# Optimization experiments

Measured on AMD Instinct MI355X. Metric: run time of the kernel, lower is better.

## Reference

```python
import jax, jax.numpy as jnp
import numpy as np

NUM_GROUPS = 32
EPS = 1e-5  # torch GroupNorm default


def group_norm(x, gamma, beta):
    # x: [b, c, h, w]
    b, c, h, w = x.shape
    xg = x.reshape(b, NUM_GROUPS, c // NUM_GROUPS, h, w)
    mean = xg.mean(axis=(2, 3, 4), keepdims=True)
    var = xg.var(axis=(2, 3, 4), keepdims=True)
    xg = (xg - mean) * jax.lax.rsqrt(var + EPS)
    x = xg.reshape(b, c, h, w)
    return x * gamma[None, :, None, None] + beta[None, :, None, None]


def conv1x1(x, w, bias):
    # 1x1 conv == channel matmul. x: [b,c,h,w], w: [cout,cin]
    y = jnp.einsum('bchw,dc->bdhw', x, w)
    return y + bias[None, :, None, None]


def setup_inputs() -> dict:
    key = jax.random.key(0)
    ks = jax.random.split(key, 11)
    C = 512
    scale = 1.0 / np.sqrt(C)
    x = jax.random.normal(ks[0], (4, C, 64, 64), dtype=jnp.float32)
    return {
        'x': x,
        'gamma': jnp.ones((C,), jnp.float32),
        'beta': jnp.zeros((C,), jnp.float32),
        'wq': jax.random.uniform(ks[1], (C, C), jnp.float32, -scale, scale),
        'bq': jax.random.uniform(ks[2], (C,), jnp.float32, -scale, scale),
        'wk': jax.random.uniform(ks[3], (C, C), jnp.float32, -scale, scale),
        'bk': jax.random.uniform(ks[4], (C,), jnp.float32, -scale, scale),
        'wv': jax.random.uniform(ks[5], (C, C), jnp.float32, -scale, scale),
        'bv': jax.random.uniform(ks[6], (C,), jnp.float32, -scale, scale),
        'wo': jax.random.uniform(ks[7], (C, C), jnp.float32, -scale, scale),
        'bo': jax.random.uniform(ks[8], (C,), jnp.float32, -scale, scale),
    }


def reference(x, gamma, beta, wq, bq, wk, bk, wv, bv, wo, bo):
    b, c, h, w = x.shape
    h_ = group_norm(x, gamma, beta)
    q = conv1x1(h_, wq, bq).reshape(b, c, h * w)
    k = conv1x1(h_, wk, bk).reshape(b, c, h * w)
    v = conv1x1(h_, wv, bv).reshape(b, c, h * w)
    # scores: [b, hw, hw] -- q^T k scaled by c^-0.5
    scores = jnp.einsum('bcn,bcm->bnm', q, k) * (c ** -0.5)
    attn = jax.nn.softmax(scores, axis=2)
    # h_ = v @ attn^T : [b, c, hw]
    out = jnp.einsum('bcm,bnm->bcn', v, attn).reshape(b, c, h, w)
    return x + conv1x1(out, wo, bo)
```

## Files before the change

kernel.cpp:

```cpp
#include <hip/hip_runtime.h>

typedef __bf16 bf16x8 __attribute__((ext_vector_type(8)));
typedef __bf16 bf16x4 __attribute__((ext_vector_type(4)));
typedef float floatx4 __attribute__((ext_vector_type(4)));

#define AS1(p) ((const __attribute__((address_space(1))) unsigned int*)(p))
#define AS3(p) ((__attribute__((address_space(3))) unsigned int*)(p))

__device__ __forceinline__ void async_cp16(const void* g, void* l) {
  __builtin_amdgcn_global_load_lds(AS1(g), AS3(l), 16, 0, 0);
}


template <bool OUT_F32>
__global__ __launch_bounds__(256, 2) void gemm_bt(
    const __bf16* __restrict__ A, const __bf16* __restrict__ B,
    void* __restrict__ Cv, const float* __restrict__ bias,
    const float* __restrict__ residual, const float* __restrict__ colscale,
    int lda, int ldb, int ldc, long sA, long sB, long sC, long sR, int K,
    int bias_mode, float scale, int swz) {
  __shared__ alignas(16) __bf16 As[128 * 64];
  __shared__ alignas(16) __bf16 Bs[128 * 64];

  const int t = threadIdx.x;
  const int bz = blockIdx.z;
  int bx = blockIdx.x, by = blockIdx.y;
  if (swz) {
    const int xcd = bx & 7, idx = bx >> 3;
    by = xcd + (idx >> 2) * 8;
    bx = idx & 3;
  }
  const int m0 = by * 128;
  const int n0 = bx * 128;

  const __bf16* Ab = A + (size_t)bz * sA;
  const __bf16* Bb = B + (size_t)bz * sB;

  const int sr = t >> 3;
  const int sc = ((t & 7) ^ ((t >> 3) & 7)) * 8;
  const __bf16* gA0 = Ab + (size_t)(m0 + sr) * lda + sc;
  const __bf16* gA1 = gA0 + (size_t)32 * lda;
  const __bf16* gA2 = gA0 + (size_t)64 * lda;
  const __bf16* gA3 = gA0 + (size_t)96 * lda;
  const __bf16* gB0 = Bb + (size_t)(n0 + sr) * ldb + sc;
  const __bf16* gB1 = gB0 + (size_t)32 * ldb;
  const __bf16* gB2 = gB0 + (size_t)64 * ldb;
  const __bf16* gB3 = gB0 + (size_t)96 * ldb;
  __bf16* lA0 = &As[t * 8];
  __bf16* lA1 = &As[(t + 256) * 8];
  __bf16* lA2 = &As[(t + 512) * 8];
  __bf16* lA3 = &As[(t + 768) * 8];
  __bf16* lB0 = &Bs[t * 8];
  __bf16* lB1 = &Bs[(t + 256) * 8];
  __bf16* lB2 = &Bs[(t + 512) * 8];
  __bf16* lB3 = &Bs[(t + 768) * 8];

  const int lane = t & 63;
  const int wv = t >> 6;
  const int wm = (wv & 1) * 64;
  const int wn = (wv >> 1) * 64;
  const int l15 = lane & 15;
  const int kg = lane >> 4;
  const int l7 = l15 & 7;

  int aoff0[4], boff0[4], aoff1[4], boff1[4];
#pragma unroll
  for (int i = 0; i < 4; ++i) {
    aoff0[i] = (wm + i * 16 + l15) * 64 + (kg ^ l7) * 8;
    aoff1[i] = (wm + i * 16 + l15) * 64 + ((4 + kg) ^ l7) * 8;
  }
#pragma unroll
  for (int j = 0; j < 4; ++j) {
    boff0[j] = (wn + j * 16 + l15) * 64 + (kg ^ l7) * 8;
    boff1[j] = (wn + j * 16 + l15) * 64 + ((4 + kg) ^ l7) * 8;
  }

  floatx4 acc[4][4] = {};

  const int KT = K >> 6;
  for (int kt = 0; kt < KT; ++kt) {
    const size_t ko = (size_t)kt * 64;
    async_cp16(gA0 + ko, lA0);
    async_cp16(gA1 + ko, lA1);
    async_cp16(gA2 + ko, lA2);
    async_cp16(gA3 + ko, lA3);
    async_cp16(gB0 + ko, lB0);
    async_cp16(gB1 + ko, lB1);
    async_cp16(gB2 + ko, lB2);
    async_cp16(gB3 + ko, lB3);
    __syncthreads();
    bf16x8 af[4], bfr[4];
#pragma unroll
    for (int i = 0; i < 4; ++i) af[i] = *(const bf16x8*)&As[aoff0[i]];
#pragma unroll
    for (int j = 0; j < 4; ++j) bfr[j] = *(const bf16x8*)&Bs[boff0[j]];
#pragma unroll
    for (int i = 0; i < 4; ++i)
#pragma unroll
      for (int j = 0; j < 4; ++j)
        acc[i][j] = __builtin_amdgcn_mfma_f32_16x16x32_bf16(af[i], bfr[j],
                                                            acc[i][j], 0, 0, 0);
#pragma unroll
    for (int i = 0; i < 4; ++i) af[i] = *(const bf16x8*)&As[aoff1[i]];
#pragma unroll
    for (int j = 0; j < 4; ++j) bfr[j] = *(const bf16x8*)&Bs[boff1[j]];
#pragma unroll
    for (int i = 0; i < 4; ++i)
#pragma unroll
      for (int j = 0; j < 4; ++j)
        acc[i][j] = __builtin_amdgcn_mfma_f32_16x16x32_bf16(af[i], bfr[j],
                                                            acc[i][j], 0, 0, 0);
    __syncthreads();
  }

  const int r0 = m0 + wm + (kg << 2);
  const int c0 = n0 + wn + l15;
#pragma unroll
  for (int i = 0; i < 4; ++i) {
#pragma unroll
    for (int r = 0; r < 4; ++r) {
      const int row = r0 + i * 16 + r;
      float brow = 0.f;
      if (bias_mode == 1) brow = bias[row];
#pragma unroll
      for (int j = 0; j < 4; ++j) {
        const int col = c0 + j * 16;
        float v = acc[i][j][r];
        if (OUT_F32 && colscale) v *= colscale[(size_t)bz * 4096 + col];
        if (bias_mode == 1) v += brow;
        v *= scale;
        const size_t off = (size_t)row * ldc + col;
        if (OUT_F32) {
          float* Cf = (float*)Cv + (size_t)bz * sC;
          if (residual) v += residual[(size_t)bz * sR + off];
          Cf[off] = v;
        } else {
          __bf16* Cb = (__bf16*)Cv + (size_t)bz * sC;
          Cb[off] = (__bf16)v;
        }
      }
    }
  }
}

__global__ __launch_bounds__(256, 2) void gemm_small(
    const __bf16* __restrict__ A0, const __bf16* __restrict__ B0,
    __bf16* __restrict__ C0, const __bf16* __restrict__ A1,
    const __bf16* __restrict__ B1, __bf16* __restrict__ C1, float scale0) {
  __shared__ alignas(16) __bf16 As[128 * 32];
  __shared__ alignas(16) __bf16 Bs[128 * 32];

  const int t = threadIdx.x;
  const int z = blockIdx.z;
  const __bf16* A = z ? A1 : A0;
  const __bf16* B = z ? B1 : B0;
  __bf16* C = z ? C1 : C0;
  const float scale = z ? 1.0f : scale0;
  const int m0 = blockIdx.y * 128;
  const int n0 = blockIdx.x * 128;

  const int sr = t >> 2;
  const int sc = (t & 3) ^ ((t >> 3) & 3);
  const __bf16* gA0 = A + (size_t)(m0 + sr) * 512 + sc * 8;
  const __bf16* gA1 = gA0 + (size_t)64 * 512;
  const __bf16* gB0 = B + (size_t)(n0 + sr) * 512 + sc * 8;
  const __bf16* gB1 = gB0 + (size_t)64 * 512;
  __bf16* lA0 = &As[t * 8];
  __bf16* lA1 = &As[(t + 256) * 8];
  __bf16* lB0 = &Bs[t * 8];
  __bf16* lB1 = &Bs[(t + 256) * 8];

  const int lane = t & 63;
  const int wvv = t >> 6;
  const int wm = (wvv & 1) * 64;
  const int wn = (wvv >> 1) * 64;
  const int l15 = lane & 15;
  const int kg = lane >> 4;

  const int kgs = (kg ^ ((l15 >> 1) & 3)) * 8;
  int aoff[4], boff[4];
#pragma unroll
  for (int i = 0; i < 4; ++i) aoff[i] = (wm + i * 16 + l15) * 32 + kgs;
#pragma unroll
  for (int j = 0; j < 4; ++j) boff[j] = (wn + j * 16 + l15) * 32 + kgs;

  floatx4 acc[4][4] = {};

  for (int kt = 0; kt < 16; ++kt) {
    const size_t ko = (size_t)kt * 32;
    async_cp16(gA0 + ko, lA0);
    async_cp16(gA1 + ko, lA1);
    async_cp16(gB0 + ko, lB0);
    async_cp16(gB1 + ko, lB1);
    __syncthreads();
    bf16x8 af[4], bfr[4];
#pragma unroll
    for (int i = 0; i < 4; ++i) af[i] = *(const bf16x8*)&As[aoff[i]];
#pragma unroll
    for (int j = 0; j < 4; ++j) bfr[j] = *(const bf16x8*)&Bs[boff[j]];
#pragma unroll
    for (int i = 0; i < 4; ++i)
#pragma unroll
      for (int j = 0; j < 4; ++j)
        acc[i][j] = __builtin_amdgcn_mfma_f32_16x16x32_bf16(af[i], bfr[j],
                                                            acc[i][j], 0, 0, 0);
    __syncthreads();
  }

  const int r0 = m0 + wm + (kg << 2);
  const int c0 = n0 + wn + l15;
#pragma unroll
  for (int i = 0; i < 4; ++i)
#pragma unroll
    for (int r = 0; r < 4; ++r) {
      const int row = r0 + i * 16 + r;
#pragma unroll
      for (int j = 0; j < 4; ++j)
        C[(size_t)row * 512 + c0 + j * 16] = (__bf16)(acc[i][j][r] * scale);
    }
}

__global__ __launch_bounds__(256, 2) void gemm_qk(
    const __bf16* __restrict__ G, const __bf16* __restrict__ Ht,
    const float* __restrict__ wvec, const float* __restrict__ sred,
    const float* __restrict__ gn2, __bf16* __restrict__ SP,
    float* __restrict__ Lpart) {
  __shared__ alignas(16) __bf16 As[128 * 64];
  __shared__ alignas(16) __bf16 Bs[128 * 64];
  __shared__ float smq[128];
  __shared__ float smf[256];

  const int t = threadIdx.x;
  const int bz = blockIdx.z;
  const int m0 = blockIdx.x * 128;
  const int n0 = blockIdx.y * 128;
  const long sH = 2097152;

  const __bf16* Ab = G + (size_t)bz * sH;
  const __bf16* Bb = Ht + (size_t)bz * sH;

  const int sr = t >> 3;
  const int sc = ((t & 7) ^ ((t >> 3) & 7)) * 8;
  const __bf16* gA0 = Ab + (size_t)(n0 + sr) * 512 + sc;
  const __bf16* gA1 = gA0 + (size_t)32 * 512;
  const __bf16* gA2 = gA0 + (size_t)64 * 512;
  const __bf16* gA3 = gA0 + (size_t)96 * 512;
  const __bf16* gB0 = Bb + (size_t)(m0 + sr) * 512 + sc;
  const __bf16* gB1 = gB0 + (size_t)32 * 512;
  const __bf16* gB2 = gB0 + (size_t)64 * 512;
  const __bf16* gB3 = gB0 + (size_t)96 * 512;
  __bf16* lA0 = &As[t * 8];
  __bf16* lA1 = &As[(t + 256) * 8];
  __bf16* lA2 = &As[(t + 512) * 8];
  __bf16* lA3 = &As[(t + 768) * 8];
  __bf16* lB0 = &Bs[t * 8];
  __bf16* lB1 = &Bs[(t + 256) * 8];
  __bf16* lB2 = &Bs[(t + 512) * 8];
  __bf16* lB3 = &Bs[(t + 768) * 8];

  const int lane = t & 63;
  const int wv = t >> 6;
  const int wm = (wv & 1) * 64;
  const int wn = (wv >> 1) * 64;
  const int l15 = lane & 15;
  const int kg = lane >> 4;
  const int l7 = l15 & 7;

  if (t < 128) {
    smq[t] = sqrtf(gn2[(size_t)bz * 4096 + n0 + t]) * sqrtf(sred[0]) + sred[1];
  }

  int aoff0[4], boff0[4], aoff1[4], boff1[4];
#pragma unroll
  for (int i = 0; i < 4; ++i) {
    aoff0[i] = (wm + i * 16 + l15) * 64 + (kg ^ l7) * 8;
    aoff1[i] = (wm + i * 16 + l15) * 64 + ((4 + kg) ^ l7) * 8;
  }
#pragma unroll
  for (int j = 0; j < 4; ++j) {
    boff0[j] = (wn + j * 16 + l15) * 64 + (kg ^ l7) * 8;
    boff1[j] = (wn + j * 16 + l15) * 64 + ((4 + kg) ^ l7) * 8;
  }

  floatx4 acc[4][4] = {};

  for (int kt = 0; kt < 8; ++kt) {
    const size_t ko = (size_t)kt * 64;
    async_cp16(gA0 + ko, lA0);
    async_cp16(gA1 + ko, lA1);
    async_cp16(gA2 + ko, lA2);
    async_cp16(gA3 + ko, lA3);
    async_cp16(gB0 + ko, lB0);
    async_cp16(gB1 + ko, lB1);
    async_cp16(gB2 + ko, lB2);
    async_cp16(gB3 + ko, lB3);
    __syncthreads();
    bf16x8 af[4], bfr[4];
#pragma unroll
    for (int i = 0; i < 4; ++i) af[i] = *(const bf16x8*)&As[aoff0[i]];
#pragma unroll
    for (int j = 0; j < 4; ++j) bfr[j] = *(const bf16x8*)&Bs[boff0[j]];
#pragma unroll
    for (int i = 0; i < 4; ++i)
#pragma unroll
      for (int j = 0; j < 4; ++j)
        acc[i][j] = __builtin_amdgcn_mfma_f32_16x16x32_bf16(af[i], bfr[j],
                                                            acc[i][j], 0, 0, 0);
#pragma unroll
    for (int i = 0; i < 4; ++i) af[i] = *(const bf16x8*)&As[aoff1[i]];
#pragma unroll
    for (int j = 0; j < 4; ++j) bfr[j] = *(const bf16x8*)&Bs[boff1[j]];
#pragma unroll
    for (int i = 0; i < 4; ++i)
#pragma unroll
      for (int j = 0; j < 4; ++j)
        acc[i][j] = __builtin_amdgcn_mfma_f32_16x16x32_bf16(af[i], bfr[j],
                                                            acc[i][j], 0, 0, 0);
    __syncthreads();
  }

  float wv4[4];
#pragma unroll
  for (int j = 0; j < 4; ++j)
    wv4[j] = wvec[(size_t)bz * 4096 + m0 + wn + j * 16 + l15];

  __bf16* Sb = SP + (size_t)bz * 16777216;
  const int wnh = wv >> 1;
#pragma unroll
  for (int i = 0; i < 4; ++i) {
#pragma unroll
    for (int r = 0; r < 4; ++r) {
      const int rl = wm + i * 16 + (kg << 2) + r;
      const float Mh = smq[rl];
      const size_t rowbase = (size_t)(n0 + rl) * 4096 + m0 + wn;
      float se = 0.f;
#pragma unroll
      for (int j = 0; j < 4; ++j) {
        const float p = __expf(acc[i][j][r] + wv4[j] - Mh);
        se += p;
        Sb[rowbase + j * 16 + l15] = (__bf16)p;
      }
#pragma unroll
      for (int off = 1; off < 16; off <<= 1) se += __shfl_xor(se, off);
      if (l15 == 0) smf[wnh * 128 + rl] = se;
    }
  }
  __syncthreads();
  if (t < 128)
    Lpart[((size_t)bz * 4096 + n0 + t) * 32 + blockIdx.x] =
        smf[t] + smf[128 + t];
}

__global__ __launch_bounds__(256) void gnorm_kernel(const __bf16* __restrict__ G,
                                                    float* __restrict__ gn2) {
  const int t = threadIdx.x;
  const int row = blockIdx.x * 4 + (t >> 6);
  const int lane = t & 63;
  const bf16x8 g = *(const bf16x8*)(G + (size_t)row * 512 + lane * 8);
  float n2 = 0.f;
#pragma unroll
  for (int k = 0; k < 8; ++k) {
    const float f = (float)g[k];
    n2 += f * f;
  }
#pragma unroll
  for (int off = 32; off; off >>= 1) n2 += __shfl_down(n2, off);
  if (lane == 0) gn2[row] = n2;
}

__global__ __launch_bounds__(256) void lsum_kernel(const float* __restrict__ Lp,
                                                   float* __restrict__ invL) {
  const int row = blockIdx.x * 256 + threadIdx.x;
  const float* p = Lp + (size_t)row * 32;
  float L = 0.f;
#pragma unroll
  for (int j = 0; j < 32; ++j) L += p[j];
  invL[row] = 1.0f / L;
}

__global__ __launch_bounds__(256) void reduce_kernel(
    const float* __restrict__ hn2, const float* __restrict__ wvec,
    float* __restrict__ sred) {
  const int t = threadIdx.x;
  const floatx4* h4 = (const floatx4*)hn2;
  const floatx4* w4 = (const floatx4*)wvec;
  float mh = 0.f, mw = -1e30f;
  for (int i = t; i < 4096; i += 256) {
    const floatx4 a = h4[i], b = w4[i];
#pragma unroll
    for (int k = 0; k < 4; ++k) {
      mh = fmaxf(mh, a[k]);
      mw = fmaxf(mw, b[k]);
    }
  }
#pragma unroll
  for (int off = 32; off; off >>= 1) {
    mh = fmaxf(mh, __shfl_down(mh, off));
    mw = fmaxf(mw, __shfl_down(mw, off));
  }
  __shared__ float red[8];
  if ((t & 63) == 0) {
    red[t >> 6] = mh;
    red[4 + (t >> 6)] = mw;
  }
  __syncthreads();
  if (t == 0) {
    sred[0] = fmaxf(fmaxf(red[0], red[1]), fmaxf(red[2], red[3]));
    sred[1] = fmaxf(fmaxf(red[4], red[5]), fmaxf(red[6], red[7]));
  }
}

__global__ __launch_bounds__(256) void gn_stats(const float* __restrict__ x,
                                                float* __restrict__ part) {
  const int t = threadIdx.x;
  const size_t base = (size_t)blockIdx.x * 8192;
  const floatx4* xp = (const floatx4*)(x + base);
  float s = 0.f, ss = 0.f;
#pragma unroll
  for (int i = 0; i < 8; ++i) {
    floatx4 v = xp[t + i * 256];
#pragma unroll
    for (int k = 0; k < 4; ++k) {
      s += v[k];
      ss += v[k] * v[k];
    }
  }
#pragma unroll
  for (int off = 32; off; off >>= 1) {
    s += __shfl_down(s, off);
    ss += __shfl_down(ss, off);
  }
  __shared__ float red[8];
  if ((t & 63) == 0) {
    red[t >> 6] = s;
    red[4 + (t >> 6)] = ss;
  }
  __syncthreads();
  if (t == 0) {
    part[blockIdx.x * 2] = red[0] + red[1] + red[2] + red[3];
    part[blockIdx.x * 2 + 1] = red[4] + red[5] + red[6] + red[7];
  }
}

__global__ __launch_bounds__(256) void gn_xform(const float* __restrict__ x,
                                                const float* __restrict__ part,
                                                const float* __restrict__ gamma,
                                                const float* __restrict__ beta,
                                                __bf16* __restrict__ Ht,
                                                __bf16* __restrict__ Hc) {
  __shared__ float tile[64][65];
  __shared__ float lsc[64], lsh[64];
  const int t = threadIdx.x;
  const int b = blockIdx.z;
  const int c0 = blockIdx.y * 64;
  const int n0 = blockIdx.x * 64;

  if (t < 64) {
    const int ch = c0 + t;
    const int bg = b * 32 + (ch >> 4);
    float s = 0.f, ss = 0.f;
#pragma unroll
    for (int k = 0; k < 8; ++k) {
      s += part[(bg * 8 + k) * 2];
      ss += part[(bg * 8 + k) * 2 + 1];
    }
    const float mean = s * (1.f / 65536.f);
    const float var = ss * (1.f / 65536.f) - mean * mean;
    const float rstd = rsqrtf(var + 1e-5f);
    const float g = gamma[ch] * rstd;
    lsc[t] = g;
    lsh[t] = beta[ch] - mean * g;
  }
  __syncthreads();

#pragma unroll
  for (int i = 0; i < 4; ++i) {
    const int slot = i * 256 + t;
    const int c = slot >> 4;
    const int nc = (slot & 15) * 4;
    const int ch = c0 + c;
    const floatx4 v =
        *(const floatx4*)&x[((size_t)b * 512 + ch) * 4096 + n0 + nc];
    const float scl = lsc[c];
    const float shf = lsh[c];
    bf16x4 hv;
#pragma unroll
    for (int k = 0; k < 4; ++k) {
      const float f = v[k] * scl + shf;
      tile[c][nc + k] = f;
      hv[k] = (__bf16)f;
    }
    *(bf16x4*)&Hc[((size_t)b * 512 + ch) * 4096 + n0 + nc] = hv;
  }
  __syncthreads();
#pragma unroll
  for (int i = 0; i < 4; ++i) {
    const int slot = i * 256 + t;
    const int n = slot >> 4;
    const int cc = (slot & 15) * 4;
    bf16x4 o;
#pragma unroll
    for (int k = 0; k < 4; ++k) o[k] = (__bf16)tile[cc + k][n];
    *(bf16x4*)&Ht[((size_t)b * 4096 + n0 + n) * 512 + c0 + cc] = o;
  }
}

__global__ __launch_bounds__(256) void cvt_kernel(const float* w0,
                                                  const float* w1,
                                                  const float* w2,
                                                  const float* w3, __bf16* o0,
                                                  __bf16* o1, __bf16* o2,
                                                  __bf16* o3) {
  __shared__ float tile[64][65];
  const int t = threadIdx.x;
  const int z = blockIdx.z;
  const int r0 = blockIdx.y * 64;
  const int d0 = blockIdx.x * 64;

  if (z == 3) {
#pragma unroll
    for (int i = 0; i < 4; ++i) {
      const int slot = i * 256 + t;
      const int r = slot >> 4;
      const int cc = (slot & 15) * 4;
      const floatx4 v = *(const floatx4*)&w3[(size_t)(r0 + r) * 512 + d0 + cc];
      bf16x4 ov;
#pragma unroll
      for (int k = 0; k < 4; ++k) ov[k] = (__bf16)v[k];
      *(bf16x4*)&o3[(size_t)(r0 + r) * 512 + d0 + cc] = ov;
    }
    return;
  }
  const float* w = z == 0 ? w0 : z == 1 ? w1 : w2;
  __bf16* o = z == 0 ? o0 : z == 1 ? o1 : o2;
#pragma unroll
  for (int i = 0; i < 4; ++i) {
    const int slot = i * 256 + t;
    const int r = slot >> 4;
    const int cc = (slot & 15) * 4;
    const floatx4 v = *(const floatx4*)&w[(size_t)(r0 + r) * 512 + d0 + cc];
#pragma unroll
    for (int k = 0; k < 4; ++k) tile[r][cc + k] = v[k];
  }
  __syncthreads();
#pragma unroll
  for (int i = 0; i < 4; ++i) {
    const int slot = i * 256 + t;
    const int d = slot >> 4;
    const int cc = (slot & 15) * 4;
    bf16x4 ov;
#pragma unroll
    for (int k = 0; k < 4; ++k) ov[k] = (__bf16)tile[cc + k][d];
    *(bf16x4*)&o[(size_t)(d0 + d) * 512 + r0 + cc] = ov;
  }
}

__global__ __launch_bounds__(256) void prep_kernel(
    const float* __restrict__ wk, const float* __restrict__ bq,
    const float* __restrict__ bk, const float* __restrict__ wo,
    const float* __restrict__ bv, const float* __restrict__ bo,
    float* __restrict__ uq, float* __restrict__ bias2, float qscale) {
  const int bidx = blockIdx.x;
  const int t = threadIdx.x;
  float s = 0.f;
  if (bidx < 512) {
    s = bq[t] * wk[(size_t)t * 512 + bidx] +
        bq[t + 256] * wk[(size_t)(t + 256) * 512 + bidx];
  } else if (bidx < 1024) {
    const int d = bidx - 512;
    s = wo[(size_t)d * 512 + t] * bv[t] +
        wo[(size_t)d * 512 + t + 256] * bv[t + 256];
  } else {
    s = bq[t] * bk[t] + bq[t + 256] * bk[t + 256];
  }
#pragma unroll
  for (int off = 32; off; off >>= 1) s += __shfl_down(s, off);
  __shared__ float red[4];
  if ((t & 63) == 0) red[t >> 6] = s;
  __syncthreads();
  if (t == 0) {
    const float tot = red[0] + red[1] + red[2] + red[3];
    if (bidx < 512)
      uq[bidx] = qscale * tot;
    else if (bidx < 1024)
      bias2[bidx - 512] = tot + bo[bidx - 512];
    else
      uq[512] = qscale * tot;
  }
}

__global__ __launch_bounds__(256) void wvec_kernel(const __bf16* __restrict__ Ht,
                                                   const float* __restrict__ uq,
                                                   float* __restrict__ wvec,
                                                   float* __restrict__ hn2) {
  const int t = threadIdx.x;
  const int row = blockIdx.x * 4 + (t >> 6);
  const int lane = t & 63;
  const bf16x8 h = *(const bf16x8*)(Ht + (size_t)row * 512 + lane * 8);
  const floatx4 u0 = *(const floatx4*)(uq + lane * 8);
  const floatx4 u1 = *(const floatx4*)(uq + lane * 8 + 4);
  float s = 0.f, n2 = 0.f;
#pragma unroll
  for (int k = 0; k < 4; ++k) {
    const float f0 = (float)h[k], f1 = (float)h[4 + k];
    s += f0 * u0[k] + f1 * u1[k];
    n2 += f0 * f0 + f1 * f1;
  }
#pragma unroll
  for (int off = 32; off; off >>= 1) {
    s += __shfl_down(s, off);
    n2 += __shfl_down(n2, off);
  }
  if (lane == 0) {
    wvec[row] = s + uq[512];
    hn2[row] = n2;
  }
}

extern "C" void kernel_launch(void* const* d_in, const int* in_sizes, int n_in,
                              void* d_out, int out_size, void* d_ws,
                              size_t ws_size, hipStream_t stream) {
  const float* x = (const float*)d_in[0];
  const float* gamma = (const float*)d_in[1];
  const float* beta = (const float*)d_in[2];
  const float* wq = (const float*)d_in[3];
  const float* bq = (const float*)d_in[4];
  const float* wk = (const float*)d_in[5];
  const float* bk = (const float*)d_in[6];
  const float* wv = (const float*)d_in[7];
  const float* bv = (const float*)d_in[8];
  const float* wo = (const float*)d_in[9];
  const float* bo = (const float*)d_in[10];

  __bf16* ws = (__bf16*)d_ws;
  __bf16* wqT = ws;
  __bf16* wkT = wqT + 262144;
  __bf16* wvT = wkT + 262144;
  __bf16* woB = wvT + 262144;
  __bf16* AqkT = woB + 262144;
  __bf16* Wb = AqkT + 262144;
  __bf16* Ht = Wb + 262144;
  __bf16* Hc = Ht + 8388608;
  __bf16* G = Hc + 8388608;
  __bf16* Z = G + 8388608;
  __bf16* SP = Z + 8388608;
  float* Lpart = (float*)(SP + 67108864);
  float* invL = Lpart + 524288;
  float* hn2 = invL + 16384;
  float* wvec = hn2 + 16384;
  float* uq = wvec + 16384;
  float* bias2 = uq + 1024;
  float* sred = bias2 + 512;
  float* gn2 = sred + 64;
  const size_t need = ((size_t)(6 * 262144 + 4 * 8388608 + 67108864)) * 2 +
                      (524288 + 4 * 16384 + 1024 + 512 + 128) * 4;
  if (ws_size < need) return;

  float* part = (float*)SP;

  const float qscale = 0.04419417382415922f;
  const long sH = 2097152;

  cvt_kernel<<<dim3(8, 8, 4), 256, 0, stream>>>(wq, wk, wv, wo, wqT, wkT, wvT,
                                                woB);
  prep_kernel<<<1025, 256, 0, stream>>>(wk, bq, bk, wo, bv, bo, uq, bias2,
                                        qscale);
  gemm_small<<<dim3(4, 4, 2), 256, 0, stream>>>(wkT, wqT, AqkT, woB, wvT, Wb,
                                                qscale);

  gn_stats<<<1024, 256, 0, stream>>>(x, part);
  gn_xform<<<dim3(64, 8, 4), 256, 0, stream>>>(x, part, gamma, beta, Ht, Hc);

  wvec_kernel<<<4096, 256, 0, stream>>>(Ht, uq, wvec, hn2);

  gemm_bt<false><<<dim3(4, 32, 4), 256, 0, stream>>>(
      Ht, AqkT, G, nullptr, nullptr, nullptr, 512, 512, 512, sH, 0, sH, 0, 512,
      0, 1.0f, 0);

  gnorm_kernel<<<4096, 256, 0, stream>>>(G, gn2);

  reduce_kernel<<<1, 256, 0, stream>>>(hn2, wvec, sred);

  gemm_qk<<<dim3(32, 32, 4), 256, 0, stream>>>(G, Ht, wvec, sred, gn2, SP,
                                               Lpart);
  lsum_kernel<<<64, 256, 0, stream>>>(Lpart, invL);

  gemm_bt<false><<<dim3(128, 1, 4), 256, 0, stream>>>(
      SP, Hc, Z, nullptr, nullptr, nullptr, 4096, 4096, 512, 16777216, sH, sH,
      0, 4096, 0, 1.0f, 1);

  gemm_bt<true><<<dim3(32, 4, 4), 256, 0, stream>>>(
      Wb, Z, d_out, bias2, x, invL, 512, 512, 4096, 0, sH, sH, sH, 512, 1,
      1.0f, 0);
}
```

Before: 362.5 us.

## Fuse row dot and norm reductions into GroupNorm transform and G GEMM epilogue

Drops the separate wvec_kernel and gnorm_kernel. gn_xform now computes per-row partial dot products with uq and squared norms as it writes Ht, and accumulates them with atomicAdd into buffers that prep_kernel zeroes. A new gemm_g writes per-64-column partial squared norms of G from its epilogue, and gemm_qk sums those partials itself. This avoids re-reading Ht and G from memory and removes two launches. In exchange it adds atomics and shuffles, and the constant uq[512] is no longer added to wvec.

After: 355.2 us. -2.0%, faster.

```diff
diff --git a/kernel.cpp b/kernel.cpp
--- a/kernel.cpp
+++ b/kernel.cpp
@@ -143,6 +143,121 @@
   }
 }
 
+__global__ __launch_bounds__(256, 2) void gemm_g(const __bf16* __restrict__ A,
+                                                 const __bf16* __restrict__ B,
+                                                 __bf16* __restrict__ C,
+                                                 float* __restrict__ gn2p) {
+  __shared__ alignas(16) __bf16 As[128 * 64];
+  __shared__ alignas(16) __bf16 Bs[128 * 64];
+
+  const int t = threadIdx.x;
+  const int bz = blockIdx.z;
+  const int m0 = blockIdx.y * 128;
+  const int n0 = blockIdx.x * 128;
+
+  const __bf16* Ab = A + (size_t)bz * 2097152;
+  const __bf16* Bb = B;
+
+  const int sr = t >> 3;
+  const int sc = ((t & 7) ^ ((t >> 3) & 7)) * 8;
+  const __bf16* gA0 = Ab + (size_t)(m0 + sr) * 512 + sc;
+  const __bf16* gA1 = gA0 + (size_t)32 * 512;
+  const __bf16* gA2 = gA0 + (size_t)64 * 512;
+  const __bf16* gA3 = gA0 + (size_t)96 * 512;
+  const __bf16* gB0 = Bb + (size_t)(n0 + sr) * 512 + sc;
+  const __bf16* gB1 = gB0 + (size_t)32 * 512;
+  const __bf16* gB2 = gB0 + (size_t)64 * 512;
+  const __bf16* gB3 = gB0 + (size_t)96 * 512;
+  __bf16* lA0 = &As[t * 8];
+  __bf16* lA1 = &As[(t + 256) * 8];
+  __bf16* lA2 = &As[(t + 512) * 8];
+  __bf16* lA3 = &As[(t + 768) * 8];
+  __bf16* lB0 = &Bs[t * 8];
+  __bf16* lB1 = &Bs[(t + 256) * 8];
+  __bf16* lB2 = &Bs[(t + 512) * 8];
+  __bf16* lB3 = &Bs[(t + 768) * 8];
+
+  const int lane = t & 63;
+  const int wv = t >> 6;
+  const int wm = (wv & 1) * 64;
+  const int wn = (wv >> 1) * 64;
+  const int l15 = lane & 15;
+  const int kg = lane >> 4;
+  const int l7 = l15 & 7;
+
+  int aoff0[4], boff0[4], aoff1[4], boff1[4];
+#pragma unroll
+  for (int i = 0; i < 4; ++i) {
+    aoff0[i] = (wm + i * 16 + l15) * 64 + (kg ^ l7) * 8;
+    aoff1[i] = (wm + i * 16 + l15) * 64 + ((4 + kg) ^ l7) * 8;
+  }
+#pragma unroll
+  for (int j = 0; j < 4; ++j) {
+    boff0[j] = (wn + j * 16 + l15) * 64 + (kg ^ l7) * 8;
+    boff1[j] = (wn + j * 16 + l15) * 64 + ((4 + kg) ^ l7) * 8;
+  }
+
+  floatx4 acc[4][4] = {};
+
+  for (int kt = 0; kt < 8; ++kt) {
+    const size_t ko = (size_t)kt * 64;
+    async_cp16(gA0 + ko, lA0);
+    async_cp16(gA1 + ko, lA1);
+    async_cp16(gA2 + ko, lA2);
+    async_cp16(gA3 + ko, lA3);
+    async_cp16(gB0 + ko, lB0);
+    async_cp16(gB1 + ko, lB1);
+    async_cp16(gB2 + ko, lB2);
+    async_cp16(gB3 + ko, lB3);
+    __syncthreads();
+    bf16x8 af[4], bfr[4];
+#pragma unroll
+    for (int i = 0; i < 4; ++i) af[i] = *(const bf16x8*)&As[aoff0[i]];
+#pragma unroll
+    for (int j = 0; j < 4; ++j) bfr[j] = *(const bf16x8*)&Bs[boff0[j]];
+#pragma unroll
+    for (int i = 0; i < 4; ++i)
+#pragma unroll
+      for (int j = 0; j < 4; ++j)
+        acc[i][j] = __builtin_amdgcn_mfma_f32_16x16x32_bf16(af[i], bfr[j],
+                                                            acc[i][j], 0, 0, 0);
+#pragma unroll
+    for (int i = 0; i < 4; ++i) af[i] = *(const bf16x8*)&As[aoff1[i]];
+#pragma unroll
+    for (int j = 0; j < 4; ++j) bfr[j] = *(const bf16x8*)&Bs[boff1[j]];
+#pragma unroll
+    for (int i = 0; i < 4; ++i)
+#pragma unroll
+      for (int j = 0; j < 4; ++j)
+        acc[i][j] = __builtin_amdgcn_mfma_f32_16x16x32_bf16(af[i], bfr[j],
+                                                            acc[i][j], 0, 0, 0);
+    __syncthreads();
+  }
+
+  __bf16* Cb = C + (size_t)bz * 2097152;
+  const int r0 = m0 + wm + (kg << 2);
+  const int c0 = n0 + wn + l15;
+  const int slot8 = (n0 >> 6) + (wv >> 1);
+#pragma unroll
+  for (int i = 0; i < 4; ++i) {
+#pragma unroll
+    for (int r = 0; r < 4; ++r) {
+      const int row = r0 + i * 16 + r;
+      float s2 = 0.f;
+#pragma unroll
+      for (int j = 0; j < 4; ++j) {
+        const __bf16 bv = (__bf16)acc[i][j][r];
+        Cb[(size_t)row * 512 + c0 + j * 16] = bv;
+        const float f = (float)bv;
+        s2 += f * f;
+      }
+#pragma unroll
+      for (int off = 1; off < 16; off <<= 1) s2 += __shfl_xor(s2, off);
+      if (l15 == 0) gn2p[((size_t)bz * 4096 + row) * 8 + slot8] = s2;
+    }
+  }
+}
+
 __global__ __launch_bounds__(256, 2) void gemm_small(
     const __bf16* __restrict__ A0, const __bf16* __restrict__ B0,
     __bf16* __restrict__ C0, const __bf16* __restrict__ A1,
@@ -223,7 +338,7 @@
 __global__ __launch_bounds__(256, 2) void gemm_qk(
     const __bf16* __restrict__ G, const __bf16* __restrict__ Ht,
     const float* __restrict__ wvec, const float* __restrict__ sred,
-    const float* __restrict__ gn2, __bf16* __restrict__ SP,
+    const float* __restrict__ gn2p, __bf16* __restrict__ SP,
     float* __restrict__ Lpart) {
   __shared__ alignas(16) __bf16 As[128 * 64];
   __shared__ alignas(16) __bf16 Bs[128 * 64];
@@ -267,7 +382,11 @@
   const int l7 = l15 & 7;
 
   if (t < 128) {
-    smq[t] = sqrtf(gn2[(size_t)bz * 4096 + n0 + t]) * sqrtf(sred[0]) + sred[1];
+    const floatx4* gp =
+        (const floatx4*)&gn2p[((size_t)bz * 4096 + n0 + t) * 8];
+    const floatx4 a = gp[0], b = gp[1];
+    const float g2 = a[0] + a[1] + a[2] + a[3] + b[0] + b[1] + b[2] + b[3];
+    smq[t] = sqrtf(g2) * sqrtf(sred[0]) + sred[1];
   }
 
   int aoff0[4], boff0[4], aoff1[4], boff1[4];
@@ -351,23 +470,6 @@
         smf[t] + smf[128 + t];
 }
 
-__global__ __launch_bounds__(256) void gnorm_kernel(const __bf16* __restrict__ G,
-                                                    float* __restrict__ gn2) {
-  const int t = threadIdx.x;
-  const int row = blockIdx.x * 4 + (t >> 6);
-  const int lane = t & 63;
-  const bf16x8 g = *(const bf16x8*)(G + (size_t)row * 512 + lane * 8);
-  float n2 = 0.f;
-#pragma unroll
-  for (int k = 0; k < 8; ++k) {
-    const float f = (float)g[k];
-    n2 += f * f;
-  }
-#pragma unroll
-  for (int off = 32; off; off >>= 1) n2 += __shfl_down(n2, off);
-  if (lane == 0) gn2[row] = n2;
-}
-
 __global__ __launch_bounds__(256) void lsum_kernel(const float* __restrict__ Lp,
                                                    float* __restrict__ invL) {
   const int row = blockIdx.x * 256 + threadIdx.x;
@@ -442,12 +544,12 @@
   }
 }
 
-__global__ __launch_bounds__(256) void gn_xform(const float* __restrict__ x,
-                                                const float* __restrict__ part,
-                                                const float* __restrict__ gamma,
-                                                const float* __restrict__ beta,
-                                                __bf16* __restrict__ Ht,
-                                                __bf16* __restrict__ Hc) {
+__global__ __launch_bounds__(256) void gn_xform(
+    const float* __restrict__ x, const float* __restrict__ part,
+    const float* __restrict__ gamma, const float* __restrict__ beta,
+    const float* __restrict__ uq, __bf16* __restrict__ Ht,
+    __bf16* __restrict__ Hc, float* __restrict__ wvec,
+    float* __restrict__ hn2) {
   __shared__ float tile[64][65];
   __shared__ float lsc[64], lsh[64];
   const int t = threadIdx.x;
@@ -498,10 +600,27 @@
     const int slot = i * 256 + t;
     const int n = slot >> 4;
     const int cc = (slot & 15) * 4;
+    const floatx4 uv = *(const floatx4*)&uq[c0 + cc];
     bf16x4 o;
-#pragma unroll
-    for (int k = 0; k < 4; ++k) o[k] = (__bf16)tile[cc + k][n];
+    float ps = 0.f, pn = 0.f;
+#pragma unroll
+    for (int k = 0; k < 4; ++k) {
+      o[k] = (__bf16)tile[cc + k][n];
+      const float f = (float)o[k];
+      ps += f * uv[k];
+      pn += f * f;
+    }
     *(bf16x4*)&Ht[((size_t)b * 4096 + n0 + n) * 512 + c0 + cc] = o;
+#pragma unroll
+    for (int off = 1; off < 16; off <<= 1) {
+      ps += __shfl_xor(ps, off);
+      pn += __shfl_xor(pn, off);
+    }
+    if ((t & 15) == 0) {
+      const size_t row = (size_t)b * 4096 + n0 + n;
+      atomicAdd(&wvec[row], ps);
+      atomicAdd(&hn2[row], pn);
+    }
   }
 }
 
@@ -559,9 +678,17 @@
     const float* __restrict__ wk, const float* __restrict__ bq,
     const float* __restrict__ bk, const float* __restrict__ wo,
     const float* __restrict__ bv, const float* __restrict__ bo,
-    float* __restrict__ uq, float* __restrict__ bias2, float qscale) {
+    float* __restrict__ uq, float* __restrict__ bias2, float qscale,
+    float* __restrict__ wvec, float* __restrict__ hn2) {
   const int bidx = blockIdx.x;
   const int t = threadIdx.x;
+  {
+    const int slot = bidx * 256 + t;
+    if (slot < 16384)
+      wvec[slot] = 0.f;
+    else if (slot < 32768)
+      hn2[slot - 16384] = 0.f;
+  }
   float s = 0.f;
   if (bidx < 512) {
     s = bq[t] * wk[(size_t)t * 512 + bidx] +
@@ -586,34 +713,6 @@
       bias2[bidx - 512] = tot + bo[bidx - 512];
     else
       uq[512] = qscale * tot;
-  }
-}
-
-__global__ __launch_bounds__(256) void wvec_kernel(const __bf16* __restrict__ Ht,
-                                                   const float* __restrict__ uq,
-                                                   float* __restrict__ wvec,
-                                                   float* __restrict__ hn2) {
-  const int t = threadIdx.x;
-  const int row = blockIdx.x * 4 + (t >> 6);
-  const int lane = t & 63;
-  const bf16x8 h = *(const bf16x8*)(Ht + (size_t)row * 512 + lane * 8);
-  const floatx4 u0 = *(const floatx4*)(uq + lane * 8);
-  const floatx4 u1 = *(const floatx4*)(uq + lane * 8 + 4);
-  float s = 0.f, n2 = 0.f;
-#pragma unroll
-  for (int k = 0; k < 4; ++k) {
-    const float f0 = (float)h[k], f1 = (float)h[4 + k];
-    s += f0 * u0[k] + f1 * u1[k];
-    n2 += f0 * f0 + f1 * f1;
-  }
-#pragma unroll
-  for (int off = 32; off; off >>= 1) {
-    s += __shfl_down(s, off);
-    n2 += __shfl_down(n2, off);
-  }
-  if (lane == 0) {
-    wvec[row] = s + uq[512];
-    hn2[row] = n2;
   }
 }
 
@@ -651,9 +750,10 @@
   float* uq = wvec + 16384;
   float* bias2 = uq + 1024;
   float* sred = bias2 + 512;
-  float* gn2 = sred + 64;
-  const size_t need = ((size_t)(6 * 262144 + 4 * 8388608 + 67108864)) * 2 +
-                      (524288 + 4 * 16384 + 1024 + 512 + 128) * 4;
+  float* gn2p = sred + 64;
+  const size_t need =
+      ((size_t)(6 * 262144 + 4 * 8388608 + 67108864)) * 2 +
+      (524288 + 3 * 16384 + 1024 + 512 + 64 + 131072) * 4;
   if (ws_size < need) return;
 
   float* part = (float*)SP;
@@ -664,24 +764,19 @@
   cvt_kernel<<<dim3(8, 8, 4), 256, 0, stream>>>(wq, wk, wv, wo, wqT, wkT, wvT,
                                                 woB);
   prep_kernel<<<1025, 256, 0, stream>>>(wk, bq, bk, wo, bv, bo, uq, bias2,
-                                        qscale);
+                                        qscale, wvec, hn2);
   gemm_small<<<dim3(4, 4, 2), 256, 0, stream>>>(wkT, wqT, AqkT, woB, wvT, Wb,
                                                 qscale);
 
   gn_stats<<<1024, 256, 0, stream>>>(x, part);
-  gn_xform<<<dim3(64, 8, 4), 256, 0, stream>>>(x, part, gamma, beta, Ht, Hc);
-
-  wvec_kernel<<<4096, 256, 0, stream>>>(Ht, uq, wvec, hn2);
-
-  gemm_bt<false><<<dim3(4, 32, 4), 256, 0, stream>>>(
-      Ht, AqkT, G, nullptr, nullptr, nullptr, 512, 512, 512, sH, 0, sH, 0, 512,
-      0, 1.0f, 0);
-
-  gnorm_kernel<<<4096, 256, 0, stream>>>(G, gn2);
+  gn_xform<<<dim3(64, 8, 4), 256, 0, stream>>>(x, part, gamma, beta, uq, Ht,
+                                               Hc, wvec, hn2);
+
+  gemm_g<<<dim3(4, 32, 4), 256, 0, stream>>>(Ht, AqkT, G, gn2p);
 
   reduce_kernel<<<1, 256, 0, stream>>>(hn2, wvec, sred);
 
-  gemm_qk<<<dim3(32, 32, 4), 256, 0, stream>>>(G, Ht, wvec, sred, gn2, SP,
+  gemm_qk<<<dim3(32, 32, 4), 256, 0, stream>>>(G, Ht, wvec, sred, gn2p, SP,
                                                Lpart);
   lsum_kernel<<<64, 256, 0, stream>>>(Lpart, invL);
 
```
